# Performance work log

Hardware: AMD Instinct MI355X
Metric: run time of the kernel (lower is better)

## Reference

```python
import jax, jax.numpy as jnp
import numpy as np

B, S, NI = 8, 1024, 1024      # batch, seq_len, n_inputs
L, H, P = 128, 128, 64        # n_latents, hidden=n_inputs//8, prototype_dim
EPS_PROTO = 1e-4              # self.epsilon
BN_EPS = 1e-5                 # torch BatchNorm1d default eps


def setup_inputs() -> dict:
    key = jax.random.key(0)
    ks = jax.random.split(key, 4)
    return {
        "x": jax.random.normal(ks[0], (B, S, NI), jnp.float32),
        "W1": jax.random.normal(ks[1], (L, H, NI), jnp.float32) * 0.02,
        "b1": jnp.zeros((L, H), jnp.float32),
        "gamma": jnp.ones((L, H), jnp.float32),
        "beta": jnp.zeros((L, H), jnp.float32),
        "run_mean": jnp.zeros((L, H), jnp.float32),
        "run_var": jnp.ones((L, H), jnp.float32),
        "W2": jax.random.normal(ks[2], (L, P, H), jnp.float32) * 0.02,
        "b2": jnp.zeros((L, P), jnp.float32),
        "prototypes": jax.random.normal(ks[3], (L, P), jnp.float32) * 0.02,
    }


def reference(x, W1, b1, gamma, beta, run_mean, run_var, W2, b2, prototypes):
    Bb, Ss, _ = x.shape
    xf = x.reshape(Bb * Ss, NI)                       # [T, NI]
    # grouped first Linear over all latents at once: [T, L, H]
    h = jnp.einsum('ti,lhi->tlh', xf, W1) + b1
    # Dropout is identity in eval; BatchNorm1d in eval mode (running stats)
    h = (h - run_mean) * jax.lax.rsqrt(run_var + BN_EPS) * gamma + beta
    h = jax.nn.relu(h)
    # grouped second Linear: [T, L, P]
    enc = jnp.einsum('tlh,lph->tlp', h, W2) + b2
    # prototype L2-distance activation
    l2s = jnp.sum((enc - prototypes) ** 2, axis=-1)   # [T, L]
    raw = jnp.log((l2s + 1.0) / (l2s + EPS_PROTO))
    act = raw / jnp.log(1.0 / EPS_PROTO) * 300.0 - 100.0
    return act.reshape(Bb, Ss, L)
```

## Files before the change

kernel.cpp:

```cpp
#include <hip/hip_runtime.h>


#define NTOK 8192
#define NI   1024
#define NL   128
#define NH   128
#define NP   64

typedef __bf16 bf16x8 __attribute__((ext_vector_type(8)));
typedef float f32x4 __attribute__((ext_vector_type(4)));
typedef int   i32x4 __attribute__((ext_vector_type(4)));

static __device__ __forceinline__ unsigned short f2bf(float f) {
  union { float f; unsigned int u; } v; v.f = f;
  const unsigned int u = v.u;
  return (unsigned short)((u + 0x7fffu + ((u >> 16) & 1u)) >> 16);
}

__global__ void cvt_f32_bf16(const float* __restrict__ in,
                             unsigned short* __restrict__ out, int n8) {
  const int i = blockIdx.x * blockDim.x + threadIdx.x;
  if (i >= n8) return;
  const float4* p = (const float4*)in;
  const float4 a = p[2 * i], b = p[2 * i + 1];
  unsigned short v[8] __attribute__((aligned(16))) = {
      f2bf(a.x), f2bf(a.y), f2bf(a.z), f2bf(a.w),
      f2bf(b.x), f2bf(b.y), f2bf(b.z), f2bf(b.w)};
  ((uint4*)out)[i] = *(const uint4*)v;
}

__global__ void quant_rows_i8_dual(const float* __restrict__ x,
                                   const float* __restrict__ w1,
                                   signed char* __restrict__ xq,
                                   signed char* __restrict__ w1q,
                                   float* __restrict__ sx,
                                   float* __restrict__ sw) {
  const int row = blockIdx.x * 4 + (threadIdx.x >> 6);
  const int lane = threadIdx.x & 63;
  const float* src;
  unsigned int* dst;
  float* sp;
  if (row < NTOK) {
    src = x + (size_t)row * 1024;
    dst = (unsigned int*)(xq + (size_t)row * 1024);
    sp  = sx + row;
  } else {
    const int r = row - NTOK;
    src = w1 + (size_t)r * 1024;
    dst = (unsigned int*)(w1q + (size_t)r * 1024);
    sp  = sw + r;
  }
  const float4* s4 = (const float4*)src;
  float4 v[4];
  float m = 0.f;
#pragma unroll
  for (int j = 0; j < 4; ++j) {
    v[j] = s4[lane + 64 * j];
    m = fmaxf(m, fmaxf(fmaxf(fabsf(v[j].x), fabsf(v[j].y)),
                       fmaxf(fabsf(v[j].z), fabsf(v[j].w))));
  }
#pragma unroll
  for (int s = 1; s < 64; s <<= 1) m = fmaxf(m, __shfl_xor(m, s));
  m = fmaxf(m, 1e-20f);
  const float inv = 127.0f / m;
  if (lane == 0) *sp = m * (1.0f / 127.0f);
#pragma unroll
  for (int j = 0; j < 4; ++j) {
    const int a = (int)rintf(fminf(127.f, fmaxf(-127.f, v[j].x * inv)));
    const int b = (int)rintf(fminf(127.f, fmaxf(-127.f, v[j].y * inv)));
    const int c = (int)rintf(fminf(127.f, fmaxf(-127.f, v[j].z * inv)));
    const int d = (int)rintf(fminf(127.f, fmaxf(-127.f, v[j].w * inv)));
    dst[lane + 64 * j] = (unsigned)(a & 255) | ((unsigned)(b & 255) << 8) |
                         ((unsigned)(c & 255) << 16) | ((unsigned)(d & 255) << 24);
  }
}

static __device__ __forceinline__ void async16(const void* g, void* l) {
  __builtin_amdgcn_global_load_lds(
      (const __attribute__((address_space(1))) unsigned int*)g,
      (__attribute__((address_space(3))) unsigned int*)l, 16, 0, 0);
}

__global__ __launch_bounds__(256, 4) void proto_fused(
    const signed char* __restrict__ xq,
    const signed char* __restrict__ w1q,
    const unsigned short* __restrict__ w2b,
    const float* __restrict__ sx,
    const float* __restrict__ sw,
    const float* __restrict__ b1,
    const float* __restrict__ gamma, const float* __restrict__ beta,
    const float* __restrict__ rmean, const float* __restrict__ rvar,
    const float* __restrict__ b2,
    const float* __restrict__ protos,
    float* __restrict__ out)
{
  __shared__ __attribute__((aligned(128))) char smem[32768];
  const int tid  = threadIdx.x;
  const int wave = tid >> 6;
  const int lane = tid & 63;
  const int l15  = lane & 15;
  const int l4   = lane >> 4;
  const int wr   = wave >> 1;
  const int wc   = wave & 1;

  const int id    = blockIdx.x;
  const int xcd   = id & 7;
  const int local = id >> 3;
  const int chunk = local >> 7;
  const int wi    = local & 127;
  const int tt    = chunk * 8 + (wi & 7);
  const int lat   = xcd * 16 + (wi >> 3);
  const int t0    = tt * 128;

  const int srow  = lane >> 3;
  const int scolb = ((lane & 7) ^ srow) * 16;

  i32x4 acc[4][4] = {};

  auto stage = [&](int ks) {
    const int k0 = ks * 128;
#pragma unroll
    for (int j = 0; j < 4; ++j) {
      const int row = wave * 32 + j * 8 + srow;
      async16(xq + (size_t)(t0 + row) * NI + k0 + scolb,
              smem + (wave * 4 + j) * 1024);
      async16(w1q + (size_t)(lat * NH + row) * NI + k0 + scolb,
              smem + 16384 + (wave * 4 + j) * 1024);
    }
  };

  stage(0);
  const int rx = l15 & 7;
  for (int ks = 0; ks < 8; ++ks) {
    __syncthreads();
#pragma unroll
    for (int kk = 0; kk < 2; ++kk) {
      const int koff = ((kk * 4 + l4) ^ rx) << 4;
      i32x4 a[4], b[4];
#pragma unroll
      for (int m = 0; m < 4; ++m)
        a[m] = *(const i32x4*)(smem + (wr * 64 + m * 16 + l15) * 128 + koff);
#pragma unroll
      for (int n = 0; n < 4; ++n)
        b[n] = *(const i32x4*)(smem + 16384 + (wc * 64 + n * 16 + l15) * 128 + koff);
#pragma unroll
      for (int m = 0; m < 4; ++m)
#pragma unroll
        for (int n = 0; n < 4; ++n)
          acc[m][n] = __builtin_amdgcn_mfma_i32_16x16x64_i8(a[m], b[n], acc[m][n], 0, 0, 0);
    }
    __syncthreads();
    if (ks + 1 < 8) stage(ks + 1);
  }

  float sxv[4][4];
#pragma unroll
  for (int m = 0; m < 4; ++m)
#pragma unroll
    for (int r = 0; r < 4; ++r)
      sxv[m][r] = sx[t0 + wr * 64 + m * 16 + l4 * 4 + r];

#pragma unroll
  for (int n = 0; n < 4; ++n) {
    const int hc = wc * 64 + n * 16 + l15;
    const int gi = lat * NH + hc;
    const float sc_ = gamma[gi] * rsqrtf(rvar[gi] + 1e-5f);
    const float Kc  = sw[gi] * sc_;
    const float Cc  = b1[gi] * sc_ + beta[gi] - rmean[gi] * sc_;
    const int cchunk = hc >> 3, cin = (hc & 7) * 2;
#pragma unroll
    for (int m = 0; m < 4; ++m)
#pragma unroll
      for (int r = 0; r < 4; ++r) {
        float v = fmaf((float)acc[m][n][r] * sxv[m][r], Kc, Cc);
        v = v > 0.f ? v : 0.f;
        const int row = wr * 64 + m * 16 + l4 * 4 + r;
        const int pbyte = row * 256 + ((cchunk ^ (l4 * 4 + r)) << 4) + cin;
        *(__bf16*)(smem + pbyte) = (__bf16)v;
      }
  }
  __syncthreads();

  f32x4 acc2[2][4] = {};
  const unsigned short* w2p = w2b + (size_t)lat * NP * NH + l15 * NH + l4 * 8;
  bf16x8 bw[4], bwn[4];
#pragma unroll
  for (int n = 0; n < 4; ++n)
    bw[n] = *(const bf16x8*)(w2p + n * 16 * NH);
#pragma unroll
  for (int kk = 0; kk < 4; ++kk) {
    if (kk < 3) {
#pragma unroll
      for (int n = 0; n < 4; ++n)
        bwn[n] = *(const bf16x8*)(w2p + n * 16 * NH + (kk + 1) * 32);
    }
    const int pcsel = kk * 4 + l4;
    bf16x8 a2[2];
#pragma unroll
    for (int m = 0; m < 2; ++m) {
      const int row = wave * 32 + m * 16 + l15;
      a2[m] = *(const bf16x8*)(smem + row * 256 + ((pcsel ^ l15) << 4));
    }
#pragma unroll
    for (int m = 0; m < 2; ++m)
#pragma unroll
      for (int n = 0; n < 4; ++n)
        acc2[m][n] = __builtin_amdgcn_mfma_f32_16x16x32_bf16(a2[m], bw[n], acc2[m][n], 0, 0, 0);
#pragma unroll
    for (int n = 0; n < 4; ++n) bw[n] = bwn[n];
  }

  float pb[4], pp[4];
#pragma unroll
  for (int n = 0; n < 4; ++n) {
    const int p = n * 16 + l15;
    pb[n] = b2[lat * NP + p];
    pp[n] = protos[lat * NP + p];
  }
  const float scale2 = 0.69314718056f * 300.0f / logf(10000.0f);
#pragma unroll
  for (int m = 0; m < 2; ++m)
#pragma unroll
    for (int r = 0; r < 4; ++r) {
      float s = 0.f;
#pragma unroll
      for (int n = 0; n < 4; ++n) {
        const float e = acc2[m][n][r] + pb[n] - pp[n];
        s += e * e;
      }
      s += __shfl_xor(s, 1);
      s += __shfl_xor(s, 2);
      s += __shfl_xor(s, 4);
      s += __shfl_xor(s, 8);
      if (l15 == 0) {
        const float a = (__log2f(s + 1.0f) - __log2f(s + 1e-4f)) * scale2 - 100.0f;
        const int trow = wave * 32 + m * 16 + l4 * 4 + r;
        out[(size_t)(t0 + trow) * NL + lat] = a;
      }
    }
}

extern "C" void kernel_launch(void* const* d_in, const int* in_sizes, int n_in,
                              void* d_out, int out_size, void* d_ws, size_t ws_size,
                              hipStream_t stream) {
  const float* x      = (const float*)d_in[0];
  const float* W1     = (const float*)d_in[1];
  const float* b1     = (const float*)d_in[2];
  const float* gamma  = (const float*)d_in[3];
  const float* beta   = (const float*)d_in[4];
  const float* rmean  = (const float*)d_in[5];
  const float* rvar   = (const float*)d_in[6];
  const float* W2     = (const float*)d_in[7];
  const float* b2     = (const float*)d_in[8];
  const float* protos = (const float*)d_in[9];
  float* out = (float*)d_out;

  char* ws = (char*)d_ws;
  signed char*    xq  = (signed char*)ws;
  signed char*    w1q = (signed char*)(ws + (size_t)8 * 1024 * 1024);
  unsigned short* w2b = (unsigned short*)(ws + (size_t)24 * 1024 * 1024);
  float*          sx  = (float*)(ws + (size_t)26 * 1024 * 1024);
  float*          sw  = (float*)(ws + (size_t)26 * 1024 * 1024 + 64 * 1024);

  quant_rows_i8_dual<<<(NTOK + NL * NH) / 4, 256, 0, stream>>>(x, W1, xq, w1q, sx, sw);
  {
    const int n8w2 = NL * NP * NH / 8;
    cvt_f32_bf16<<<(n8w2 + 255) / 256, 256, 0, stream>>>(W2, w2b, n8w2);
  }

  proto_fused<<<dim3(8192), 256, 0, stream>>>(xq, w1q, w2b, sx, sw, b1, gamma, beta,
                                              rmean, rvar, b2, protos, out);
}
```

Before: 239.0 us.

## Double-buffer int8 GEMM K-loop in LDS and stage W2 through shared memory

Shared memory grows from 32KB to 64KB so the next K-slice of x and W1 can be loaded asynchronously while MFMAs run on the current slice, removing one barrier per iteration. The MFMA block is raised in priority with s_setprio. W2 is now brought into LDS asynchronously during the epilogue, replacing per-lane global loads in the second GEMM. The larger LDS footprint lowers occupancy, so launch bounds drop from 4 to 2 blocks per SM, which reduces latency hiding across blocks.

```diff
diff --git a/kernel.cpp b/kernel.cpp
--- a/kernel.cpp
+++ b/kernel.cpp
@@ -81,7 +81,7 @@
       (__attribute__((address_space(3))) unsigned int*)l, 16, 0, 0);
 }
 
-__global__ __launch_bounds__(256, 4) void proto_fused(
+__global__ __launch_bounds__(256, 2) void proto_fused(
     const signed char* __restrict__ xq,
     const signed char* __restrict__ w1q,
     const unsigned short* __restrict__ w2b,
@@ -94,7 +94,7 @@
     const float* __restrict__ protos,
     float* __restrict__ out)
 {
-  __shared__ __attribute__((aligned(128))) char smem[32768];
+  __shared__ __attribute__((aligned(128))) char smem[65536];
   const int tid  = threadIdx.x;
   const int wave = tid >> 6;
   const int lane = tid & 63;
@@ -115,42 +115,68 @@
   const int srow  = lane >> 3;
   const int scolb = ((lane & 7) ^ srow) * 16;
 
+  const signed char* aB[4];
+  const signed char* bB[4];
+  int dA[4], dB[4];
+#pragma unroll
+  for (int j = 0; j < 4; ++j) {
+    const int row = wave * 32 + j * 8 + srow;
+    aB[j] = xq  + (size_t)(t0 + row) * NI + scolb;
+    bB[j] = w1q + (size_t)(lat * NH + row) * NI + scolb;
+    dA[j] = (wave * 4 + j) * 1024;
+    dB[j] = 16384 + (wave * 4 + j) * 1024;
+  }
+
   i32x4 acc[4][4] = {};
 
-  auto stage = [&](int ks) {
-    const int k0 = ks * 128;
+  auto stage = [&](int buf, int ks) {
+    const int k0   = ks * 128;
+    const int bofs = buf * 32768;
 #pragma unroll
     for (int j = 0; j < 4; ++j) {
-      const int row = wave * 32 + j * 8 + srow;
-      async16(xq + (size_t)(t0 + row) * NI + k0 + scolb,
-              smem + (wave * 4 + j) * 1024);
-      async16(w1q + (size_t)(lat * NH + row) * NI + k0 + scolb,
-              smem + 16384 + (wave * 4 + j) * 1024);
+      async16(aB[j] + k0, smem + bofs + dA[j]);
+      async16(bB[j] + k0, smem + bofs + dB[j]);
     }
   };
 
-  stage(0);
+  stage(0, 0);
+  __syncthreads();
   const int rx = l15 & 7;
+  int buf = 0;
   for (int ks = 0; ks < 8; ++ks) {
-    __syncthreads();
+    if (ks + 1 < 8) stage(buf ^ 1, ks + 1);
+    const char* Ab = smem + buf * 32768;
+    const char* Bb = Ab + 16384;
+    i32x4 a[2][4], b[2][4];
 #pragma unroll
     for (int kk = 0; kk < 2; ++kk) {
       const int koff = ((kk * 4 + l4) ^ rx) << 4;
-      i32x4 a[4], b[4];
 #pragma unroll
       for (int m = 0; m < 4; ++m)
-        a[m] = *(const i32x4*)(smem + (wr * 64 + m * 16 + l15) * 128 + koff);
+        a[kk][m] = *(const i32x4*)(Ab + (wr * 64 + m * 16 + l15) * 128 + koff);
 #pragma unroll
       for (int n = 0; n < 4; ++n)
-        b[n] = *(const i32x4*)(smem + 16384 + (wc * 64 + n * 16 + l15) * 128 + koff);
+        b[kk][n] = *(const i32x4*)(Bb + (wc * 64 + n * 16 + l15) * 128 + koff);
+    }
+    __builtin_amdgcn_s_setprio(1);
+#pragma unroll
+    for (int kk = 0; kk < 2; ++kk)
 #pragma unroll
       for (int m = 0; m < 4; ++m)
 #pragma unroll
         for (int n = 0; n < 4; ++n)
-          acc[m][n] = __builtin_amdgcn_mfma_i32_16x16x64_i8(a[m], b[n], acc[m][n], 0, 0, 0);
-    }
+          acc[m][n] = __builtin_amdgcn_mfma_i32_16x16x64_i8(a[kk][m], b[kk][n], acc[m][n], 0, 0, 0);
+    __builtin_amdgcn_s_setprio(0);
     __syncthreads();
-    if (ks + 1 < 8) stage(ks + 1);
+    buf ^= 1;
+  }
+
+#pragma unroll
+  for (int i = 0; i < 4; ++i) {
+    const int r = wave * 4 + i * 16 + l4;
+    const int c = (lane & 15) ^ (r & 15);
+    async16(w2b + (size_t)lat * NP * NH + r * NH + c * 8,
+            smem + 32768 + (wave * 64 + i * 256) * 16);
   }
 
   float sxv[4][4];
@@ -182,32 +208,25 @@
   __syncthreads();
 
   f32x4 acc2[2][4] = {};
-  const unsigned short* w2p = w2b + (size_t)lat * NP * NH + l15 * NH + l4 * 8;
-  bf16x8 bw[4], bwn[4];
-#pragma unroll
-  for (int n = 0; n < 4; ++n)
-    bw[n] = *(const bf16x8*)(w2p + n * 16 * NH);
 #pragma unroll
   for (int kk = 0; kk < 4; ++kk) {
-    if (kk < 3) {
-#pragma unroll
-      for (int n = 0; n < 4; ++n)
-        bwn[n] = *(const bf16x8*)(w2p + n * 16 * NH + (kk + 1) * 32);
-    }
     const int pcsel = kk * 4 + l4;
-    bf16x8 a2[2];
+    bf16x8 a2[2], bw[4];
 #pragma unroll
     for (int m = 0; m < 2; ++m) {
       const int row = wave * 32 + m * 16 + l15;
       a2[m] = *(const bf16x8*)(smem + row * 256 + ((pcsel ^ l15) << 4));
     }
 #pragma unroll
+    for (int n = 0; n < 4; ++n) {
+      const int rp = n * 16 + l15;
+      bw[n] = *(const bf16x8*)(smem + 32768 + rp * 256 + ((pcsel ^ l15) << 4));
+    }
+#pragma unroll
     for (int m = 0; m < 2; ++m)
 #pragma unroll
       for (int n = 0; n < 4; ++n)
         acc2[m][n] = __builtin_amdgcn_mfma_f32_16x16x32_bf16(a2[m], bw[n], acc2[m][n], 0, 0, 0);
-#pragma unroll
-    for (int n = 0; n < 4; ++n) bw[n] = bwn[n];
   }
 
   float pb[4], pp[4];
```

Result: no change. 239.9 us (+0.4%).
